# Kernel optimization log

Hardware: AMD Instinct MI355X
Metric: run time of the kernel (lower is better)

## Reference

```python
import jax, jax.numpy as jnp
import numpy as np

V, E, T_MAX, H, L = 20000, 384, 512, 8, 8
D = E // H  # head size 48
FF = 4 * E


def setup_inputs() -> dict:
    key = jax.random.key(0)
    ks = jax.random.split(key, 24)
    B, T = 16, 512
    s = 0.02
    return {
        "index": jax.random.randint(ks[0], (B, T), 0, V, dtype=jnp.int64),
        "targets": jax.random.randint(ks[1], (B, T), 0, V, dtype=jnp.int64),
        "tok_emb": s * jax.random.normal(ks[2], (V, E), jnp.float32),
        "pos_emb": s * jax.random.normal(ks[3], (T_MAX, E), jnp.float32),
        "Wq": s * jax.random.normal(ks[4], (L, E, H, D), jnp.float32),
        "bq": jnp.zeros((L, H, D), jnp.float32),
        "Wk": s * jax.random.normal(ks[5], (L, E, H, D), jnp.float32),
        "bk": jnp.zeros((L, H, D), jnp.float32),
        "Wv": s * jax.random.normal(ks[6], (L, E, H, D), jnp.float32),
        "bv": jnp.zeros((L, H, D), jnp.float32),
        "Wo": s * jax.random.normal(ks[7], (L, E, E), jnp.float32),
        "bo": jnp.zeros((L, E), jnp.float32),
        "ln1_g": jnp.ones((L, E), jnp.float32),
        "ln1_b": jnp.zeros((L, E), jnp.float32),
        "ln2_g": jnp.ones((L, E), jnp.float32),
        "ln2_b": jnp.zeros((L, E), jnp.float32),
        "W1": s * jax.random.normal(ks[8], (L, E, FF), jnp.float32),
        "b1": jnp.zeros((L, FF), jnp.float32),
        "W2": s * jax.random.normal(ks[9], (L, FF, E), jnp.float32),
        "b2": jnp.zeros((L, E), jnp.float32),
        "lnf_g": jnp.ones((E,), jnp.float32),
        "lnf_b": jnp.zeros((E,), jnp.float32),
        "lm_b": jnp.zeros((V,), jnp.float32),
    }


def layernorm(x, g, b, eps=1e-5):
    mu = jnp.mean(x, axis=-1, keepdims=True)
    var = jnp.var(x, axis=-1, keepdims=True)
    return (x - mu) * jax.lax.rsqrt(var + eps) * g + b


def reference(index, targets, tok_emb, pos_emb, Wq, bq, Wk, bk, Wv, bv, Wo, bo,
              ln1_g, ln1_b, ln2_g, ln2_b, W1, b1, W2, b2, lnf_g, lnf_b, lm_b):
    B, T = index.shape
    x = tok_emb[index] + pos_emb[:T]  # [B,T,E]
    causal = jnp.tril(jnp.ones((T, T), bool))
    scale = D ** -0.5
    for l in range(L):
        h = layernorm(x, ln1_g[l], ln1_b[l])
        q = jnp.einsum('bte,ehd->bthd', h, Wq[l]) + bq[l]
        k = jnp.einsum('bte,ehd->bthd', h, Wk[l]) + bk[l]
        v = jnp.einsum('bte,ehd->bthd', h, Wv[l]) + bv[l]
        scores = jnp.einsum('bqhd,bkhd->bhqk', q, k) * scale
        scores = jnp.where(causal, scores, -jnp.inf)
        w = jax.nn.softmax(scores, axis=-1)
        attn = jnp.einsum('bhqk,bkhd->bqhd', w, v).reshape(B, T, E)
        x = x + attn @ Wo[l] + bo[l]
        h2 = layernorm(x, ln2_g[l], ln2_b[l])
        ff = jax.nn.gelu(h2 @ W1[l] + b1[l], approximate=False) @ W2[l] + b2[l]
        x = x + ff
    x = layernorm(x, lnf_g, lnf_b)
    logits = x @ tok_emb.T + lm_b  # tied weights
    logits = logits.reshape(B * T, V)
    logp = jax.nn.log_softmax(logits, axis=-1)
    loss = -jnp.mean(jnp.take_along_axis(logp, targets.reshape(-1, 1), axis=-1))
    return logits, loss
```

## Files before the change

### kernel.cpp

```cpp
#include <hip/hip_runtime.h>
#include <hip/hip_bf16.h>
#include <math.h>

#define M_ROWS 8192
#define E_DIM 384
#define FF_DIM 1536
#define V_DIM 20000
#define VPAD 20096
#define N_LAYER 8
#define QK_SCALE 0.14433756729740643f
#define PSTRIDE 320
#define NPART 314

typedef __bf16 bf16x8 __attribute__((ext_vector_type(8)));
typedef short  s16x8  __attribute__((ext_vector_type(8)));
typedef float  f32x4  __attribute__((ext_vector_type(4)));
typedef __hip_bfloat16 bf16_t;

__device__ __forceinline__ void gl2lds16(const void* g, void* l) {
    __builtin_amdgcn_global_load_lds((const __attribute__((address_space(1))) void*)g,
                                     (__attribute__((address_space(3))) void*)l, 16, 0, 0);
}
__device__ __forceinline__ unsigned short bf16bits(float v) {
    return __builtin_bit_cast(unsigned short, __float2bfloat16(v));
}

__global__ __launch_bounds__(256) void tconv_kernel(
    const float* __restrict__ in, bf16_t* __restrict__ out,
    int K, int N, int outRows, int rowoff)
{
    __shared__ float tile[32][33];
    const int n0 = blockIdx.x * 32, k0 = blockIdx.y * 32;
    const float* ip = in + (size_t)blockIdx.z * K * N;
    bf16_t* op = out + (size_t)blockIdx.z * outRows * K;
    const int tx = threadIdx.x & 31, ty = threadIdx.x >> 5;
#pragma unroll
    for (int i = 0; i < 32; i += 8)
        tile[ty + i][tx] = ip[(size_t)(k0 + ty + i) * N + n0 + tx];
    __syncthreads();
#pragma unroll
    for (int i = 0; i < 32; i += 8)
        op[(size_t)(rowoff + n0 + ty + i) * K + k0 + tx] = __float2bfloat16(tile[tx][ty + i]);
}

__global__ __launch_bounds__(256) void tokconv_kernel(
    const float* __restrict__ tok, bf16_t* __restrict__ out)
{
    const size_t total = (size_t)VPAD * E_DIM;
    for (size_t i = blockIdx.x * 256ull + threadIdx.x; i < total; i += gridDim.x * 256ull) {
        int row = (int)(i / E_DIM);
        int col = (int)(i - (size_t)row * E_DIM);
        float v = (row < V_DIM) ? tok[(size_t)row * E_DIM + col] : 0.f;
        out[i] = __float2bfloat16(v);
    }
}

__global__ __launch_bounds__(256) void bqkv_kernel(
    const float* __restrict__ bq, const float* __restrict__ bk,
    const float* __restrict__ bv, float* __restrict__ o)
{
    int i = blockIdx.x * 256 + threadIdx.x;
    if (i < N_LAYER * 1152) {
        int l = i / 1152, c = i - l * 1152;
        float v = (c < 384) ? bq[l * 384 + c] : (c < 768) ? bk[l * 384 + c - 384] : bv[l * 384 + c - 768];
        o[i] = v;
    }
}

__global__ __launch_bounds__(256) void embed_kernel(
    const int* __restrict__ idx, const float* __restrict__ tok,
    const float* __restrict__ pos, float* __restrict__ x)
{
    int row = blockIdx.x * 4 + (threadIdx.x >> 6);
    int lane = threadIdx.x & 63;
    int t = row & 511;
    int id = idx[row];
    const float* tr = tok + (size_t)id * E_DIM;
    const float* pr = pos + (size_t)t * E_DIM;
    float* xr = x + (size_t)row * E_DIM;
#pragma unroll
    for (int i = 0; i < 6; i++) { int c = lane + i * 64; xr[c] = tr[c] + pr[c]; }
}

__global__ __launch_bounds__(256) void ln_kernel(
    const float* __restrict__ x, const float* __restrict__ g,
    const float* __restrict__ b, bf16_t* __restrict__ out)
{
    int row = blockIdx.x * 4 + (threadIdx.x >> 6);
    int lane = threadIdx.x & 63;
    const float* xr = x + (size_t)row * E_DIM;
    float vals[6];
    float s = 0.f;
#pragma unroll
    for (int i = 0; i < 6; i++) { vals[i] = xr[lane + i * 64]; s += vals[i]; }
#pragma unroll
    for (int off = 1; off < 64; off <<= 1) s += __shfl_xor(s, off);
    float mu = s * (1.f / E_DIM);
    float sq = 0.f;
#pragma unroll
    for (int i = 0; i < 6; i++) { float d = vals[i] - mu; sq += d * d; }
#pragma unroll
    for (int off = 1; off < 64; off <<= 1) sq += __shfl_xor(sq, off);
    float rstd = rsqrtf(sq * (1.f / E_DIM) + 1e-5f);
    bf16_t* orow = out + (size_t)row * E_DIM;
#pragma unroll
    for (int i = 0; i < 6; i++) {
        int c = lane + i * 64;
        orow[c] = __float2bfloat16((vals[i] - mu) * rstd * g[c] + b[c]);
    }
}

template <int MODE, int MREP>
__global__ __launch_bounds__(256) void gemm_kernel(
    const bf16_t* __restrict__ A, const bf16_t* __restrict__ Bt,
    const float* __restrict__ bias, void* __restrict__ Cv, void* __restrict__ C2,
    int Ncols, int K)
{
    constexpr int BMR = MREP * 32;
    constexpr int ASH = BMR * 32;
    constexpr int BUFSH = ASH + 4096;
    constexpr int NLD = MREP / 2 + 2;
    __shared__ __align__(16) short smem[3 * BUFSH];
    const int t = threadIdx.x;
    const int w = t >> 6, lane = t & 63;
    const int wm = w >> 1, wn = w & 1;
    const int bm = (MODE == 3 ? blockIdx.x : blockIdx.y) * BMR;
    const int bn = (MODE == 3 ? blockIdx.y : blockIdx.x) * 128;

    f32x4 acc[MREP][4];
#pragma unroll
    for (int m = 0; m < MREP; m++)
#pragma unroll
        for (int n = 0; n < 4; n++)
            acc[m][n] = (f32x4){0.f, 0.f, 0.f, 0.f};

    const int lg = lane >> 4;
    const int ll = lane & 15;
    const int nt = K / 32;

    auto stagef = [&](int kt, int buf) {
        short* sA = smem + buf * BUFSH;
        short* sB = sA + ASH;
#pragma unroll
        for (int i = 0; i < MREP / 2; i++) {
            int li = i * 256 + t;
            int g = li >> (MREP == 4 ? 7 : 6);
            int row = li & (BMR - 1);
            gl2lds16(A + (size_t)(bm + row) * K + kt + g * 8,
                     sA + (size_t)(i * 256 + w * 64) * 8);
        }
#pragma unroll
        for (int i = 0; i < 2; i++) {
            int li = i * 256 + t;
            gl2lds16(Bt + (size_t)(bn + (li & 127)) * K + kt + (li >> 7) * 8,
                     sB + (size_t)(i * 256 + w * 64) * 8);
        }
    };

    stagef(0, 0);
    stagef(32, 1);

    for (int tt = 0; tt < nt; ++tt) {
        if (tt + 2 < nt) {
            stagef((tt + 2) * 32, (tt + 2) % 3);
            asm volatile("s_waitcnt vmcnt(%0)" :: "n"(2 * NLD) : "memory");
        } else if (tt + 1 < nt) {
            asm volatile("s_waitcnt vmcnt(%0)" :: "n"(NLD) : "memory");
        } else {
            asm volatile("s_waitcnt vmcnt(0)" ::: "memory");
        }
        __builtin_amdgcn_s_barrier();

        const short* sA = smem + (tt % 3) * BUFSH;
        const short* sB = sA + ASH;
        bf16x8 af[MREP], bfr[4];
#pragma unroll
        for (int m = 0; m < MREP; m++)
            af[m] = __builtin_bit_cast(bf16x8,
                *(const s16x8*)&sA[(lg * BMR + wm * (BMR / 2) + m * 16 + ll) * 8]);
#pragma unroll
        for (int n = 0; n < 4; n++)
            bfr[n] = __builtin_bit_cast(bf16x8,
                *(const s16x8*)&sB[(lg * 128 + wn * 64 + n * 16 + ll) * 8]);
#pragma unroll
        for (int m = 0; m < MREP; m++)
#pragma unroll
            for (int n = 0; n < 4; n++)
                acc[m][n] = __builtin_amdgcn_mfma_f32_16x16x32_bf16(bfr[n], af[m], acc[m][n], 0, 0, 0);

        __builtin_amdgcn_s_barrier();
    }

    const int rowm0 = bm + wm * (BMR / 2) + ll;
    const int coln0 = bn + wn * 64 + lg * 4;

    if constexpr (MODE == 4) {
        if (bn < 768) {
            bf16_t* qkvb = (bf16_t*)Cv;
            const float sc = (bn >= 384) ? 1.f : QK_SCALE;
#pragma unroll
            for (int n = 0; n < 4; n++) {
                const int coln = coln0 + n * 16;
                const float4 b4 = *(const float4*)&bias[coln];
#pragma unroll
                for (int m = 0; m < MREP; m++) {
                    const int row = rowm0 + m * 16;
                    ushort4 pk;
                    pk.x = bf16bits((acc[m][n][0] + b4.x) * sc);
                    pk.y = bf16bits((acc[m][n][1] + b4.y) * sc);
                    pk.z = bf16bits((acc[m][n][2] + b4.z) * sc);
                    pk.w = bf16bits((acc[m][n][3] + b4.w) * sc);
                    *(ushort4*)&qkvb[(size_t)row * 1152 + coln] = pk;
                }
            }
        } else {
            bf16_t* vtb = (bf16_t*)C2;
            const int cc0 = coln0 - 768;
#pragma unroll
            for (int n = 0; n < 4; n++) {
                const float4 b4 = *(const float4*)&bias[coln0 + n * 16];
#pragma unroll
                for (int m = 0; m < MREP; m++) {
                    const int row = rowm0 + m * 16;
                    const int bb = row >> 9, tt2 = row & 511;
                    bf16_t* vb = vtb + (size_t)bb * 384 * 512 + tt2;
                    vb[(size_t)(cc0 + n * 16 + 0) * 512] = __float2bfloat16(acc[m][n][0] + b4.x);
                    vb[(size_t)(cc0 + n * 16 + 1) * 512] = __float2bfloat16(acc[m][n][1] + b4.y);
                    vb[(size_t)(cc0 + n * 16 + 2) * 512] = __float2bfloat16(acc[m][n][2] + b4.z);
                    vb[(size_t)(cc0 + n * 16 + 3) * 512] = __float2bfloat16(acc[m][n][3] + b4.w);
                }
            }
        }
    } else if constexpr (MODE == 1) {
        float* C = (float*)Cv;
#pragma unroll
        for (int n = 0; n < 4; n++) {
            const int coln = coln0 + n * 16;
            const float4 b4 = *(const float4*)&bias[coln];
#pragma unroll
            for (int m = 0; m < MREP; m++) {
                const int row = rowm0 + m * 16;
                float4 cv = *(float4*)&C[(size_t)row * Ncols + coln];
                cv.x += acc[m][n][0] + b4.x;
                cv.y += acc[m][n][1] + b4.y;
                cv.z += acc[m][n][2] + b4.z;
                cv.w += acc[m][n][3] + b4.w;
                *(float4*)&C[(size_t)row * Ncols + coln] = cv;
            }
        }
    } else if constexpr (MODE == 2) {
        bf16_t* O = (bf16_t*)Cv;
#pragma unroll
        for (int n = 0; n < 4; n++) {
            const int coln = coln0 + n * 16;
            const float4 b4 = *(const float4*)&bias[coln];
#pragma unroll
            for (int m = 0; m < MREP; m++) {
                const int row = rowm0 + m * 16;
                float v0 = acc[m][n][0] + b4.x, v1 = acc[m][n][1] + b4.y;
                float v2 = acc[m][n][2] + b4.z, v3 = acc[m][n][3] + b4.w;
                v0 = 0.5f * v0 * (1.f + erff(v0 * 0.70710678118654752f));
                v1 = 0.5f * v1 * (1.f + erff(v1 * 0.70710678118654752f));
                v2 = 0.5f * v2 * (1.f + erff(v2 * 0.70710678118654752f));
                v3 = 0.5f * v3 * (1.f + erff(v3 * 0.70710678118654752f));
                ushort4 pk;
                pk.x = bf16bits(v0); pk.y = bf16bits(v1);
                pk.z = bf16bits(v2); pk.w = bf16bits(v3);
                *(ushort4*)&O[(size_t)row * Ncols + coln] = pk;
            }
        }
    } else if constexpr (MODE == 3) {
        float* C = (float*)Cv;
        float* pbuf = (float*)C2;
        const int ptile = blockIdx.y * 2 + wn;
#pragma unroll
        for (int m = 0; m < MREP; m++) {
            const int row = rowm0 + m * 16;
            float se = 0.f;
#pragma unroll
            for (int n = 0; n < 4; n++) {
                const int coln = coln0 + n * 16;
                if (coln + 3 < Ncols) {
                    const float4 b4 = *(const float4*)&bias[coln];
                    f32x4 v;
                    v[0] = acc[m][n][0] + b4.x;
                    v[1] = acc[m][n][1] + b4.y;
                    v[2] = acc[m][n][2] + b4.z;
                    v[3] = acc[m][n][3] + b4.w;
                    __builtin_nontemporal_store(v, (f32x4*)&C[(size_t)row * Ncols + coln]);
                    se += __expf(v[0]) + __expf(v[1]) + __expf(v[2]) + __expf(v[3]);
                } else {
#pragma unroll
                    for (int e = 0; e < 4; e++) {
                        int col = coln + e;
                        if (col < Ncols) {
                            float v = acc[m][n][e] + bias[col];
                            __builtin_nontemporal_store(v, &C[(size_t)row * Ncols + col]);
                            se += __expf(v);
                        }
                    }
                }
            }
            se += __shfl_xor(se, 16);
            se += __shfl_xor(se, 32);
            if (lg == 0)
                __builtin_nontemporal_store(se, &pbuf[(size_t)row * PSTRIDE + ptile]);
        }
    }
}

__global__ __launch_bounds__(256) void attn_kernel(
    const bf16_t* __restrict__ qkvb, const bf16_t* __restrict__ vt,
    bf16_t* __restrict__ o)
{
    const int qt = blockIdx.x, bh = blockIdx.y;
    const int b = bh >> 3, h = bh & 7;
    __shared__ unsigned short psm[4608];
    const int tid = threadIdx.x;
    const int w = tid >> 6, lane = tid & 63;
    const int ll = lane & 15, g = lane >> 4;
    const int q0 = qt * 64;
    const int q_abs = q0 + ll * 4 + w;

    const bf16_t* qrow = qkvb + (size_t)(b * 512 + q_abs) * 1152 + h * 48;
    bf16x8 qf0 = __builtin_bit_cast(bf16x8, *(const s16x8*)(qrow + g * 8));
    bf16x8 qf1 = {};
    if (g < 2) qf1 = __builtin_bit_cast(bf16x8, *(const s16x8*)(qrow + 32 + g * 8));

    f32x4 oacc[3];
#pragma unroll
    for (int df = 0; df < 3; df++) oacc[df] = (f32x4){0.f, 0.f, 0.f, 0.f};
    float mrun = -1e30f, ssum = 0.f;

    const bf16_t* kptr = qkvb + (size_t)b * 512 * 1152 + 384 + h * 48;
    const bf16_t* vptr = vt + (size_t)(bh >> 3) * 384 * 512 + (size_t)(bh & 7) * 48 * 512;
    const int ntiles = 2 * (qt + 1);

    auto loadK = [&](int kbase, bf16x8& c00, bf16x8& c01, bf16x8& c10, bf16x8& c11) {
        const bf16_t* kr0 = kptr + (size_t)(kbase + ll) * 1152;
        const bf16_t* kr1 = kptr + (size_t)(kbase + 16 + ll) * 1152;
        c00 = __builtin_bit_cast(bf16x8, *(const s16x8*)(kr0 + g * 8));
        c10 = __builtin_bit_cast(bf16x8, *(const s16x8*)(kr1 + g * 8));
        bf16x8 z = {};
        c01 = (g < 2) ? __builtin_bit_cast(bf16x8, *(const s16x8*)(kr0 + 32 + g * 8)) : z;
        c11 = (g < 2) ? __builtin_bit_cast(bf16x8, *(const s16x8*)(kr1 + 32 + g * 8)) : z;
    };

    auto doTile = [&](int kbase, int parity,
                      const bf16x8& c00, const bf16x8& c01, const bf16x8& c10, const bf16x8& c11,
                      bool pf, int nbase,
                      bf16x8& n00, bf16x8& n01, bf16x8& n10, bf16x8& n11) {
        bf16x8 vf[3];
#pragma unroll
        for (int df = 0; df < 3; df++)
            vf[df] = __builtin_bit_cast(bf16x8,
                *(const s16x8*)(vptr + (size_t)(df * 16 + ll) * 512 + kbase + g * 8));
        if (pf) loadK(nbase, n00, n01, n10, n11);

        f32x4 sfr[2];
        {
            f32x4 z0 = {0.f, 0.f, 0.f, 0.f};
            z0 = __builtin_amdgcn_mfma_f32_16x16x32_bf16(c00, qf0, z0, 0, 0, 0);
            z0 = __builtin_amdgcn_mfma_f32_16x16x32_bf16(c01, qf1, z0, 0, 0, 0);
            sfr[0] = z0;
            f32x4 z1 = {0.f, 0.f, 0.f, 0.f};
            z1 = __builtin_amdgcn_mfma_f32_16x16x32_bf16(c10, qf0, z1, 0, 0, 0);
            z1 = __builtin_amdgcn_mfma_f32_16x16x32_bf16(c11, qf1, z1, 0, 0, 0);
            sfr[1] = z1;
        }

        float p[8];
        float tmax = -1e30f;
#pragma unroll
        for (int f = 0; f < 2; f++)
#pragma unroll
            for (int j = 0; j < 4; j++) {
                int key = kbase + f * 16 + g * 4 + j;
                float sv = sfr[f][j];
                sv = (key > q_abs) ? -1e30f : sv;
                p[f * 4 + j] = sv;
                tmax = fmaxf(tmax, sv);
            }
        tmax = fmaxf(tmax, __shfl_xor(tmax, 16));
        tmax = fmaxf(tmax, __shfl_xor(tmax, 32));
        float mnew = fmaxf(mrun, tmax);
        float corr = __expf(mrun - mnew);
        float psum = 0.f;
#pragma unroll
        for (int i = 0; i < 8; i++) { p[i] = __expf(p[i] - mnew); psum += p[i]; }
        psum += __shfl_xor(psum, 16);
        psum += __shfl_xor(psum, 32);
        ssum = ssum * corr + psum;
        mrun = mnew;
#pragma unroll
        for (int df = 0; df < 3; df++)
#pragma unroll
            for (int j = 0; j < 4; j++) oacc[df][j] *= corr;

        const int pbase = (w * 2 + parity) * 576;
#pragma unroll
        for (int f = 0; f < 2; f++)
#pragma unroll
            for (int j = 0; j < 4; j++)
                psm[pbase + (f * 16 + g * 4 + j) * 18 + ll] = bf16bits(p[f * 4 + j]);
        s16x8 pr;
#pragma unroll
        for (int i = 0; i < 8; i++)
            pr[i] = (short)psm[pbase + (g * 8 + i) * 18 + ll];
        bf16x8 pfr = __builtin_bit_cast(bf16x8, pr);
#pragma unroll
        for (int df = 0; df < 3; df++)
            oacc[df] = __builtin_amdgcn_mfma_f32_16x16x32_bf16(vf[df], pfr, oacc[df], 0, 0, 0);
    };

    bf16x8 kA0, kA1, kA2, kA3, kB0, kB1, kB2, kB3;
    loadK(0, kA0, kA1, kA2, kA3);
    for (int kt = 0; kt < ntiles; kt += 2) {
        doTile(kt * 32, 0, kA0, kA1, kA2, kA3,
               true, (kt + 1) * 32, kB0, kB1, kB2, kB3);
        doTile((kt + 1) * 32, 1, kB0, kB1, kB2, kB3,
               (kt + 2) < ntiles, (kt + 2) * 32, kA0, kA1, kA2, kA3);
    }

    float inv = 1.f / ssum;
    bf16_t* orow = o + (size_t)(b * 512 + q_abs) * 384 + h * 48;
#pragma unroll
    for (int df = 0; df < 3; df++) {
        ushort4 pk;
        pk.x = bf16bits(oacc[df][0] * inv);
        pk.y = bf16bits(oacc[df][1] * inv);
        pk.z = bf16bits(oacc[df][2] * inv);
        pk.w = bf16bits(oacc[df][3] * inv);
        *(ushort4*)&orow[df * 16 + g * 4] = pk;
    }
}

__global__ __launch_bounds__(256) void loss_row2_kernel(
    const float* __restrict__ pbuf, const float* __restrict__ logits,
    const int* __restrict__ targets, float* __restrict__ rowloss)
{
    int row = blockIdx.x * 4 + (threadIdx.x >> 6);
    int lane = threadIdx.x & 63;
    const float* pr = pbuf + (size_t)row * PSTRIDE;
    float s = 0.f;
    for (int i = lane; i < NPART; i += 64) s += pr[i];
#pragma unroll
    for (int off = 1; off < 64; off <<= 1) s += __shfl_xor(s, off);
    if (lane == 0) {
        int tgt = targets[row];
        rowloss[row] = logf(s) - logits[(size_t)row * V_DIM + tgt];
    }
}

__global__ __launch_bounds__(256) void loss_reduce_kernel(
    const float* __restrict__ rowloss, float* __restrict__ out)
{
    int t = threadIdx.x;
    __shared__ float red[4];
    float s = 0.f;
    for (int i = t; i < M_ROWS; i += 256) s += rowloss[i];
#pragma unroll
    for (int off = 1; off < 64; off <<= 1) s += __shfl_xor(s, off);
    if ((t & 63) == 0) red[t >> 6] = s;
    __syncthreads();
    if (t == 0) out[0] = (red[0] + red[1] + red[2] + red[3]) * (1.f / M_ROWS);
}

extern "C" void kernel_launch(void* const* d_in, const int* in_sizes, int n_in,
                              void* d_out, int out_size, void* d_ws, size_t ws_size,
                              hipStream_t stream)
{
    const int*   index   = (const int*)d_in[0];
    const int*   targets = (const int*)d_in[1];
    const float* tok_emb = (const float*)d_in[2];
    const float* pos_emb = (const float*)d_in[3];
    const float* Wq = (const float*)d_in[4];
    const float* bq = (const float*)d_in[5];
    const float* Wk = (const float*)d_in[6];
    const float* bk = (const float*)d_in[7];
    const float* Wv = (const float*)d_in[8];
    const float* bv = (const float*)d_in[9];
    const float* Wo = (const float*)d_in[10];
    const float* bo = (const float*)d_in[11];
    const float* ln1_g = (const float*)d_in[12];
    const float* ln1_b = (const float*)d_in[13];
    const float* ln2_g = (const float*)d_in[14];
    const float* ln2_b = (const float*)d_in[15];
    const float* W1 = (const float*)d_in[16];
    const float* b1 = (const float*)d_in[17];
    const float* W2 = (const float*)d_in[18];
    const float* b2 = (const float*)d_in[19];
    const float* lnf_g = (const float*)d_in[20];
    const float* lnf_b = (const float*)d_in[21];
    const float* lm_b  = (const float*)d_in[22];

    float* out = (float*)d_out;
    char* wsb = (char*)d_ws;

    float*  x     = (float*)(wsb + 0);
    bf16_t* hbuf  = (bf16_t*)(wsb + 12582912);
    bf16_t* obuf  = (bf16_t*)(wsb + 18874368);
    bf16_t* qkvb  = (bf16_t*)(wsb + 25165824);
    bf16_t* vtb   = (bf16_t*)(wsb + 44040192);
    bf16_t* ffmid = (bf16_t*)(wsb + 18874368);
    float*  pbuf  = (float*)(wsb + 25165824);
    bf16_t* tokb  = (bf16_t*)(wsb + 50331648);
    bf16_t* qkvw  = (bf16_t*)(wsb + 65765376);
    bf16_t* wo_t  = (bf16_t*)(wsb + 72843264);
    bf16_t* w1_t  = (bf16_t*)(wsb + 75202560);
    bf16_t* w2_t  = (bf16_t*)(wsb + 84639744);
    float*  bqkv  = (float*)(wsb + 94076928);
    float*  rowloss = (float*)(wsb + 94113792);

    tokconv_kernel<<<2048, 256, 0, stream>>>(tok_emb, tokb);
    tconv_kernel<<<dim3(12, 12, 8), 256, 0, stream>>>(Wq, qkvw, 384, 384, 1152, 0);
    tconv_kernel<<<dim3(12, 12, 8), 256, 0, stream>>>(Wk, qkvw, 384, 384, 1152, 384);
    tconv_kernel<<<dim3(12, 12, 8), 256, 0, stream>>>(Wv, qkvw, 384, 384, 1152, 768);
    tconv_kernel<<<dim3(12, 12, 8), 256, 0, stream>>>(Wo, wo_t, 384, 384, 384, 0);
    tconv_kernel<<<dim3(48, 12, 8), 256, 0, stream>>>(W1, w1_t, 384, 1536, 1536, 0);
    tconv_kernel<<<dim3(12, 48, 8), 256, 0, stream>>>(W2, w2_t, 1536, 384, 384, 0);
    bqkv_kernel<<<36, 256, 0, stream>>>(bq, bk, bv, bqkv);

    embed_kernel<<<2048, 256, 0, stream>>>(index, tok_emb, pos_emb, x);

    for (int l = 0; l < N_LAYER; l++) {
        const bf16_t* qkvw_l = qkvw + (size_t)l * 1152 * 384;
        const float*  bqkv_l = bqkv + l * 1152;
        ln_kernel<<<2048, 256, 0, stream>>>(x, ln1_g + l * E_DIM, ln1_b + l * E_DIM, hbuf);
        gemm_kernel<4, 4><<<dim3(9, 64), 256, 0, stream>>>(
            hbuf, qkvw_l, bqkv_l, qkvb, vtb, 1152, 384);
        attn_kernel<<<dim3(8, 128), 256, 0, stream>>>(qkvb, vtb, obuf);
        gemm_kernel<1, 2><<<dim3(3, 128), 256, 0, stream>>>(
            obuf, wo_t + (size_t)l * 384 * 384, bo + l * E_DIM, x, nullptr, 384, 384);
        ln_kernel<<<2048, 256, 0, stream>>>(x, ln2_g + l * E_DIM, ln2_b + l * E_DIM, hbuf);
        gemm_kernel<2, 4><<<dim3(12, 64), 256, 0, stream>>>(
            hbuf, w1_t + (size_t)l * 1536 * 384, b1 + l * FF_DIM, ffmid, nullptr, 1536, 384);
        gemm_kernel<1, 2><<<dim3(3, 128), 256, 0, stream>>>(
            ffmid, w2_t + (size_t)l * 384 * 1536, b2 + l * E_DIM, x, nullptr, 384, 1536);
    }

    ln_kernel<<<2048, 256, 0, stream>>>(x, lnf_g, lnf_b, hbuf);
    gemm_kernel<3, 4><<<dim3(64, 157), 256, 0, stream>>>(
        hbuf, tokb, lm_b, out, pbuf, V_DIM, 384);

    loss_row2_kernel<<<2048, 256, 0, stream>>>(pbuf, out, targets, rowloss);
    loss_reduce_kernel<<<1, 256, 0, stream>>>(rowloss, out + (size_t)M_ROWS * V_DIM);
}
```

Measured before the change: 1.836 ms.

## Fuse residual-add GEMMs with following LayerNorm and vectorize token conversion

Adds a gemm_ln_kernel in which each block owns 32 full rows of all 384 output columns. It computes the Wo or W2 projection, adds bias and the residual, writes x, then performs LayerNorm in the epilogue and emits bf16 input for the next GEMM. This removes the separate ln_kernel launches and the extra passes over x, though each block now loops over three column tiles and the grid drops to 256 blocks, which may lower parallelism. The tok_emb bf16 conversion is also rewritten to use 8-wide vector loads and stores.

```diff
diff --git a/kernel.cpp b/kernel.cpp
--- a/kernel.cpp
+++ b/kernel.cpp
@@ -46,12 +46,21 @@
 __global__ __launch_bounds__(256) void tokconv_kernel(
     const float* __restrict__ tok, bf16_t* __restrict__ out)
 {
-    const size_t total = (size_t)VPAD * E_DIM;
-    for (size_t i = blockIdx.x * 256ull + threadIdx.x; i < total; i += gridDim.x * 256ull) {
-        int row = (int)(i / E_DIM);
-        int col = (int)(i - (size_t)row * E_DIM);
-        float v = (row < V_DIM) ? tok[(size_t)row * E_DIM + col] : 0.f;
-        out[i] = __float2bfloat16(v);
+    const int total = VPAD * 48;
+    for (int idx = blockIdx.x * 256 + threadIdx.x; idx < total; idx += gridDim.x * 256) {
+        int row = idx / 48, gc = idx - row * 48;
+        int col = gc * 8;
+        s16x8 pk = {};
+        if (row < V_DIM) {
+            const float* tp = tok + (size_t)row * E_DIM + col;
+            float4 f0 = *(const float4*)tp;
+            float4 f1 = *(const float4*)(tp + 4);
+            pk[0] = (short)bf16bits(f0.x); pk[1] = (short)bf16bits(f0.y);
+            pk[2] = (short)bf16bits(f0.z); pk[3] = (short)bf16bits(f0.w);
+            pk[4] = (short)bf16bits(f1.x); pk[5] = (short)bf16bits(f1.y);
+            pk[6] = (short)bf16bits(f1.z); pk[7] = (short)bf16bits(f1.w);
+        }
+        *(s16x8*)&out[(size_t)row * E_DIM + col] = pk;
     }
 }
 
@@ -229,23 +238,6 @@
                     vb[(size_t)(cc0 + n * 16 + 2) * 512] = __float2bfloat16(acc[m][n][2] + b4.z);
                     vb[(size_t)(cc0 + n * 16 + 3) * 512] = __float2bfloat16(acc[m][n][3] + b4.w);
                 }
-            }
-        }
-    } else if constexpr (MODE == 1) {
-        float* C = (float*)Cv;
-#pragma unroll
-        for (int n = 0; n < 4; n++) {
-            const int coln = coln0 + n * 16;
-            const float4 b4 = *(const float4*)&bias[coln];
-#pragma unroll
-            for (int m = 0; m < MREP; m++) {
-                const int row = rowm0 + m * 16;
-                float4 cv = *(float4*)&C[(size_t)row * Ncols + coln];
-                cv.x += acc[m][n][0] + b4.x;
-                cv.y += acc[m][n][1] + b4.y;
-                cv.z += acc[m][n][2] + b4.z;
-                cv.w += acc[m][n][3] + b4.w;
-                *(float4*)&C[(size_t)row * Ncols + coln] = cv;
             }
         }
     } else if constexpr (MODE == 2) {
@@ -309,6 +301,125 @@
     }
 }
 
+__global__ __launch_bounds__(256) void gemm_ln_kernel(
+    const bf16_t* __restrict__ A, const bf16_t* __restrict__ Bt,
+    const float* __restrict__ bias, float* __restrict__ x,
+    const float* __restrict__ ln_g, const float* __restrict__ ln_b,
+    bf16_t* __restrict__ outH, int K)
+{
+    constexpr int BUFSH = 1024 + 4096;
+    __shared__ __align__(16) short smem[3 * BUFSH];
+    __shared__ float red[2][16][2][2];
+    const int t = threadIdx.x;
+    const int w = t >> 6, lane = t & 63;
+    const int wm = w >> 1, wn = w & 1;
+    const int lg = lane >> 4, ll = lane & 15;
+    const int bm = blockIdx.x * 32;
+    const int nt = K / 32;
+
+    f32x4 acc[3][4];
+#pragma unroll
+    for (int n3 = 0; n3 < 3; n3++)
+#pragma unroll
+        for (int n = 0; n < 4; n++)
+            acc[n3][n] = (f32x4){0.f, 0.f, 0.f, 0.f};
+
+    auto stagef = [&](int ntile, int kt, int buf) {
+        short* sA = smem + buf * BUFSH;
+        short* sB = sA + 1024;
+        if (t < 128) {
+            gl2lds16(A + (size_t)(bm + (t & 31)) * K + kt + (t >> 5) * 8, sA + t * 8);
+        }
+#pragma unroll
+        for (int i = 0; i < 2; i++) {
+            int li = i * 256 + t;
+            gl2lds16(Bt + (size_t)(ntile * 128 + (li & 127)) * K + kt + (li >> 7) * 8,
+                     sB + (size_t)(i * 256 + w * 64) * 8);
+        }
+    };
+
+    for (int n3 = 0; n3 < 3; n3++) {
+        stagef(n3, 0, 0);
+        stagef(n3, 32, 1);
+        for (int tt = 0; tt < nt; ++tt) {
+            if (tt + 2 < nt) {
+                stagef(n3, (tt + 2) * 32, (tt + 2) % 3);
+                if (w < 2) asm volatile("s_waitcnt vmcnt(6)" ::: "memory");
+                else       asm volatile("s_waitcnt vmcnt(4)" ::: "memory");
+            } else if (tt + 1 < nt) {
+                if (w < 2) asm volatile("s_waitcnt vmcnt(3)" ::: "memory");
+                else       asm volatile("s_waitcnt vmcnt(2)" ::: "memory");
+            } else {
+                asm volatile("s_waitcnt vmcnt(0)" ::: "memory");
+            }
+            __builtin_amdgcn_s_barrier();
+
+            const short* sA = smem + (tt % 3) * BUFSH;
+            const short* sB = sA + 1024;
+            bf16x8 af = __builtin_bit_cast(bf16x8,
+                *(const s16x8*)&sA[(lg * 32 + wm * 16 + ll) * 8]);
+            bf16x8 bfr[4];
+#pragma unroll
+            for (int n = 0; n < 4; n++)
+                bfr[n] = __builtin_bit_cast(bf16x8,
+                    *(const s16x8*)&sB[(lg * 128 + wn * 64 + n * 16 + ll) * 8]);
+#pragma unroll
+            for (int n = 0; n < 4; n++)
+                acc[n3][n] = __builtin_amdgcn_mfma_f32_16x16x32_bf16(bfr[n], af, acc[n3][n], 0, 0, 0);
+
+            __builtin_amdgcn_s_barrier();
+        }
+    }
+
+    const int row = bm + wm * 16 + ll;
+    float* xrow = x + (size_t)row * 384;
+    float sum = 0.f, ssq = 0.f;
+#pragma unroll
+    for (int n3 = 0; n3 < 3; n3++) {
+#pragma unroll
+        for (int n = 0; n < 4; n++) {
+            const int coln = n3 * 128 + wn * 64 + lg * 4 + n * 16;
+            const float4 b4 = *(const float4*)&bias[coln];
+            float4 xv = *(float4*)&xrow[coln];
+            acc[n3][n][0] += b4.x + xv.x;
+            acc[n3][n][1] += b4.y + xv.y;
+            acc[n3][n][2] += b4.z + xv.z;
+            acc[n3][n][3] += b4.w + xv.w;
+            float4 nx;
+            nx.x = acc[n3][n][0]; nx.y = acc[n3][n][1];
+            nx.z = acc[n3][n][2]; nx.w = acc[n3][n][3];
+            *(float4*)&xrow[coln] = nx;
+            sum += nx.x + nx.y + nx.z + nx.w;
+            ssq += nx.x * nx.x + nx.y * nx.y + nx.z * nx.z + nx.w * nx.w;
+        }
+    }
+    sum += __shfl_xor(sum, 16); sum += __shfl_xor(sum, 32);
+    ssq += __shfl_xor(ssq, 16); ssq += __shfl_xor(ssq, 32);
+    if (lg == 0) { red[wm][ll][wn][0] = sum; red[wm][ll][wn][1] = ssq; }
+    __syncthreads();
+    float tsum = red[wm][ll][0][0] + red[wm][ll][1][0];
+    float tssq = red[wm][ll][0][1] + red[wm][ll][1][1];
+    float mu = tsum * (1.f / 384.f);
+    float rstd = rsqrtf(tssq * (1.f / 384.f) - mu * mu + 1e-5f);
+
+    bf16_t* hrow = outH + (size_t)row * 384;
+#pragma unroll
+    for (int n3 = 0; n3 < 3; n3++) {
+#pragma unroll
+        for (int n = 0; n < 4; n++) {
+            const int coln = n3 * 128 + wn * 64 + lg * 4 + n * 16;
+            const float4 g4 = *(const float4*)&ln_g[coln];
+            const float4 bb4 = *(const float4*)&ln_b[coln];
+            ushort4 pk;
+            pk.x = bf16bits((acc[n3][n][0] - mu) * rstd * g4.x + bb4.x);
+            pk.y = bf16bits((acc[n3][n][1] - mu) * rstd * g4.y + bb4.y);
+            pk.z = bf16bits((acc[n3][n][2] - mu) * rstd * g4.z + bb4.z);
+            pk.w = bf16bits((acc[n3][n][3] - mu) * rstd * g4.w + bb4.w);
+            *(ushort4*)&hrow[coln] = pk;
+        }
+    }
+}
+
 __global__ __launch_bounds__(256) void attn_kernel(
     const bf16_t* __restrict__ qkvb, const bf16_t* __restrict__ vt,
     bf16_t* __restrict__ o)
@@ -333,7 +444,7 @@
     float mrun = -1e30f, ssum = 0.f;
 
     const bf16_t* kptr = qkvb + (size_t)b * 512 * 1152 + 384 + h * 48;
-    const bf16_t* vptr = vt + (size_t)(bh >> 3) * 384 * 512 + (size_t)(bh & 7) * 48 * 512;
+    const bf16_t* vptr = vt + (size_t)b * 384 * 512 + (size_t)h * 48 * 512;
     const int ntiles = 2 * (qt + 1);
 
     auto loadK = [&](int kbase, bf16x8& c00, bf16x8& c01, bf16x8& c10, bf16x8& c11) {
@@ -434,6 +545,7 @@
         *(ushort4*)&orow[df * 16 + g * 4] = pk;
     }
 }
+
 
 __global__ __launch_bounds__(256) void loss_row2_kernel(
     const float* __restrict__ pbuf, const float* __restrict__ logits,
@@ -522,24 +634,26 @@
     bqkv_kernel<<<36, 256, 0, stream>>>(bq, bk, bv, bqkv);
 
     embed_kernel<<<2048, 256, 0, stream>>>(index, tok_emb, pos_emb, x);
+    ln_kernel<<<2048, 256, 0, stream>>>(x, ln1_g, ln1_b, hbuf);
 
     for (int l = 0; l < N_LAYER; l++) {
         const bf16_t* qkvw_l = qkvw + (size_t)l * 1152 * 384;
         const float*  bqkv_l = bqkv + l * 1152;
-        ln_kernel<<<2048, 256, 0, stream>>>(x, ln1_g + l * E_DIM, ln1_b + l * E_DIM, hbuf);
         gemm_kernel<4, 4><<<dim3(9, 64), 256, 0, stream>>>(
             hbuf, qkvw_l, bqkv_l, qkvb, vtb, 1152, 384);
         attn_kernel<<<dim3(8, 128), 256, 0, stream>>>(qkvb, vtb, obuf);
-        gemm_kernel<1, 2><<<dim3(3, 128), 256, 0, stream>>>(
-            obuf, wo_t + (size_t)l * 384 * 384, bo + l * E_DIM, x, nullptr, 384, 384);
-        ln_kernel<<<2048, 256, 0, stream>>>(x, ln2_g + l * E_DIM, ln2_b + l * E_DIM, hbuf);
+        gemm_ln_kernel<<<256, 256, 0, stream>>>(
+            obuf, wo_t + (size_t)l * 384 * 384, bo + l * E_DIM, x,
+            ln2_g + l * E_DIM, ln2_b + l * E_DIM, hbuf, 384);
         gemm_kernel<2, 4><<<dim3(12, 64), 256, 0, stream>>>(
             hbuf, w1_t + (size_t)l * 1536 * 384, b1 + l * FF_DIM, ffmid, nullptr, 1536, 384);
-        gemm_kernel<1, 2><<<dim3(3, 128), 256, 0, stream>>>(
-            ffmid, w2_t + (size_t)l * 384 * 1536, b2 + l * E_DIM, x, nullptr, 384, 1536);
-    }
-
-    ln_kernel<<<2048, 256, 0, stream>>>(x, lnf_g, lnf_b, hbuf);
+        const float* ng = (l < 7) ? ln1_g + (l + 1) * E_DIM : lnf_g;
+        const float* nb = (l < 7) ? ln1_b + (l + 1) * E_DIM : lnf_b;
+        gemm_ln_kernel<<<256, 256, 0, stream>>>(
+            ffmid, w2_t + (size_t)l * 384 * 1536, b2 + l * E_DIM, x,
+            ng, nb, hbuf, 1536);
+    }
+
     gemm_kernel<3, 4><<<dim3(64, 157), 256, 0, stream>>>(
         hbuf, tokb, lm_b, out, pbuf, V_DIM, 384);
 
```

Measured after the change: 2.273 ms. +23.8%, slower.
